# Kernel tuning notes

Hardware: AMD Instinct MI355X
Metric: run time of the kernel (lower is better)

Reference implementation:

```python
import jax, jax.numpy as jnp
import numpy as np

B, L, D = 2, 2048, 512
DI, N, K, R = 1024, 16, 4, 32  # d_inner=2*d_model, d_state, d_conv, dt_rank=ceil(512/16)
CK = 31   # conformer depthwise kernel
DFF = 2048  # feedforward_factor * d_hidden

def _ln(h, g, b):
    m = h.mean(-1, keepdims=True)
    v = ((h - m) ** 2).mean(-1, keepdims=True)
    return (h - m) * jax.lax.rsqrt(v + 1e-5) * g + b

def _dwconv(h, w, b, pad):
    # h: [B,L,C], w: [C,1,K] depthwise kernel
    y = jax.lax.conv_general_dilated(h.transpose(0, 2, 1), w, (1,), [pad],
                                     feature_group_count=h.shape[-1],
                                     dimension_numbers=('NCH', 'OIH', 'NCH'))
    return y.transpose(0, 2, 1) + b

def setup_inputs():
    key = jax.random.key(0)
    ks = jax.random.split(key, 16)
    nrm = lambda k, s, sc=0.02: jax.random.normal(k, s, jnp.float32) * sc
    return {
        'x': jax.random.normal(ks[0], (B, L, D), jnp.float32),
        'ln_g': jnp.ones(D), 'ln_b': jnp.zeros(D),
        'W_in': nrm(ks[1], (D, 2 * DI)),
        'conv_w': nrm(ks[2], (DI, 1, K), 0.1), 'conv_b': jnp.zeros(DI),
        'W_x': nrm(ks[3], (DI, R + 2 * N)),
        'W_dt': nrm(ks[4], (R, DI), 0.1), 'b_dt': nrm(ks[5], (DI,), 0.1),
        'A_log': jnp.log(jnp.broadcast_to(jnp.arange(1, N + 1, dtype=jnp.float32), (DI, N))),
        'Dp': jnp.ones(DI),
        'W_out': nrm(ks[6], (DI, D)),
        'cm_ln_g': jnp.ones(D), 'cm_ln_b': jnp.zeros(D),
        'cm_pw1_w': nrm(ks[7], (D, 2 * D)), 'cm_pw1_b': jnp.zeros(2 * D),
        'cm_dw_w': nrm(ks[8], (D, 1, CK), 0.1), 'cm_dw_b': jnp.zeros(D),
        'cm_pw2_w': nrm(ks[9], (D, D)), 'cm_pw2_b': jnp.zeros(D),
        'ff_W1': nrm(ks[10], (D, DFF)), 'ff_b1': jnp.zeros(DFF),
        'ff_W2': nrm(ks[11], (DFF, D)), 'ff_b2': jnp.zeros(D),
    }

def _forward(x, ln_g, ln_b, W_in, conv_w, conv_b, W_x, W_dt, b_dt, A_log, Dp, W_out,
             cm_ln_g, cm_ln_b, cm_pw1_w, cm_pw1_b, cm_dw_w, cm_dw_b, cm_pw2_w, cm_pw2_b,
             ff_W1, ff_b1, ff_W2, ff_b2):
    # --- pre LayerNorm ---
    h = _ln(x, ln_g, ln_b)
    # --- Mamba block ---
    xz = h @ W_in                       # [B,L,2*DI]
    xi, z = xz[..., :DI], xz[..., DI:]
    xc = jax.nn.silu(_dwconv(xi, conv_w, conv_b, (K - 1, 0)))  # causal depthwise conv
    dbl = xc @ W_x                      # [B,L,R+2N]
    dt, Bm, Cm = dbl[..., :R], dbl[..., R:R + N], dbl[..., R + N:]
    delta = jax.nn.softplus(dt @ W_dt + b_dt)           # [B,L,DI]
    A = -jnp.exp(A_log)                                  # [DI,N]
    dA = jnp.exp(delta[..., None] * A)                   # [B,L,DI,N]
    dBu = (delta * xc)[..., None] * Bm[:, :, None, :]    # [B,L,DI,N]
    def step(hs, inp):
        a, bu, c = inp
        hs = a * hs + bu                                 # [B,DI,N]
        return hs, jnp.einsum('bdn,bn->bd', hs, c)
    h0 = jnp.zeros((x.shape[0], DI, N), x.dtype)
    _, ys = jax.lax.scan(step, h0, (dA.transpose(1, 0, 2, 3), dBu.transpose(1, 0, 2, 3), Cm.transpose(1, 0, 2)))
    y = ys.transpose(1, 0, 2) + Dp * xc
    y = y * jax.nn.silu(z)
    m = y @ W_out                                        # [B,L,D]
    # --- Conformer-style conv module (residual) ---
    c = _ln(m, cm_ln_g, cm_ln_b)
    c = c @ cm_pw1_w + cm_pw1_b
    a_, g_ = jnp.split(c, 2, axis=-1)
    c = a_ * jax.nn.sigmoid(g_)  # GLU
    c = jax.nn.silu(_dwconv(c, cm_dw_w, cm_dw_b, ((CK - 1) // 2, (CK - 1) // 2)))
    c = c @ cm_pw2_w + cm_pw2_b
    m = m + c
    # --- post LayerNorm (shared params) + FFN (residual) ---
    f = _ln(m, ln_g, ln_b)
    out = f + (jax.nn.gelu(f @ ff_W1 + ff_b1) @ ff_W2 + ff_b2)
    return out

def reference(x, ln_g, ln_b, W_in, conv_w, conv_b, W_x, W_dt, b_dt, A_log, Dp, W_out,
              cm_ln_g, cm_ln_b, cm_pw1_w, cm_pw1_b, cm_dw_w, cm_dw_b, cm_pw2_w, cm_pw2_b,
              ff_W1, ff_b1, ff_W2, ff_b2):
    return _forward(x, ln_g, ln_b, W_in, conv_w, conv_b, W_x, W_dt, b_dt, A_log, Dp, W_out,
                    cm_ln_g, cm_ln_b, cm_pw1_w, cm_pw1_b, cm_dw_w, cm_dw_b, cm_pw2_w, cm_pw2_b,
                    ff_W1, ff_b1, ff_W2, ff_b2)
```

## Files before the change

### kernel.cpp

```cpp
#include <hip/hip_runtime.h>
#include <hip/hip_bf16.h>
#include <math.h>

#define Bc   2
#define Lc   2048
#define Dc   512
#define DIc  1024
#define Nc   16
#define Kc   4
#define Rc   32
#define CKc  31
#define DFFc 2048
#define Mrows (Bc*Lc)
#define CHUNK  32
#define NCHUNK 64

typedef __hip_bfloat16 bf16;
typedef short bf16x8 __attribute__((ext_vector_type(8)));
typedef float f32x4  __attribute__((ext_vector_type(4)));

__device__ __forceinline__ float sigmoidf_(float x){ return 1.f/(1.f+expf(-x)); }
__device__ __forceinline__ float siluf_(float x){ return x*sigmoidf_(x); }
__device__ __forceinline__ float softplusf_(float x){ return fmaxf(x,0.f)+log1pf(expf(-fabsf(x))); }
__device__ __forceinline__ float geluf_(float x){
    float x3 = x*x*x;
    return 0.5f*x*(1.f+tanhf(0.7978845608028654f*(x+0.044715f*x3)));
}

__device__ __forceinline__ void gload16(const void* g, void* l) {
    __builtin_amdgcn_global_load_lds((const __attribute__((address_space(1))) void*)g,
                                     (__attribute__((address_space(3))) void*)l, 16, 0, 0);
}

template<bool WF, bool WB>
__global__ void ln_kernel(const float* __restrict__ in, const float* __restrict__ g,
                          const float* __restrict__ bb, float* __restrict__ outf,
                          bf16* __restrict__ outb, int D) {
    int row = blockIdx.x;
    const float* x = in + (size_t)row * D;
    float s = 0.f, s2 = 0.f;
    for (int i = threadIdx.x; i < D; i += blockDim.x) { float v = x[i]; s += v; s2 += v*v; }
    #pragma unroll
    for (int off = 32; off; off >>= 1) { s += __shfl_down(s, off); s2 += __shfl_down(s2, off); }
    __shared__ float sh[2][4];
    int wave = threadIdx.x >> 6, lane = threadIdx.x & 63;
    if (lane == 0) { sh[0][wave] = s; sh[1][wave] = s2; }
    __syncthreads();
    if (threadIdx.x == 0) {
        float ts = 0.f, ts2 = 0.f;
        int nw = blockDim.x >> 6;
        for (int w = 0; w < nw; ++w) { ts += sh[0][w]; ts2 += sh[1][w]; }
        sh[0][0] = ts; sh[1][0] = ts2;
    }
    __syncthreads();
    float mean = sh[0][0] / D;
    float var  = sh[1][0] / D - mean*mean;
    float rstd = rsqrtf(var + 1e-5f);
    for (int i = threadIdx.x; i < D; i += blockDim.x) {
        float v = (x[i]-mean)*rstd*g[i] + bb[i];
        if (WF) outf[(size_t)row*D + i] = v;
        if (WB) outb[(size_t)row*D + i] = __float2bfloat16(v);
    }
}

struct WtPack {
    const float* W[8];
    bf16* Wt[8];
    int K[8];
    int N[8];
    int start[9];
};

__global__ void wtrans_all(WtPack p) {
    __shared__ float t[32][33];
    int tb = blockIdx.x;
    int wi = 0;
    #pragma unroll
    for (int i = 0; i < 7; ++i) if (tb >= p.start[i+1]) wi = i+1;
    int lt = tb - p.start[wi];
    int K = p.K[wi], N = p.N[wi];
    int ntx = N >> 5;
    int bx = lt % ntx, by = lt / ntx;
    const float* W = p.W[wi];
    bf16* Wt = p.Wt[wi];
    int tx = threadIdx.x, ty = threadIdx.y;
    #pragma unroll
    for (int i = 0; i < 32; i += 8)
        t[ty+i][tx] = W[(size_t)(by*32+ty+i)*N + bx*32+tx];
    __syncthreads();
    #pragma unroll
    for (int i = 0; i < 32; i += 8)
        Wt[(size_t)(bx*32+ty+i)*K + by*32+tx] = __float2bfloat16(t[tx][ty+i]);
}

template<int BM, int BN, int SPLITK, int ZSEL, int ACT, bool BIAS, bool RES, bool WF32, bool WBF16>
__global__ __launch_bounds__(256) void mgemm(const bf16* __restrict__ A, int lda,
                                             const bf16* __restrict__ Wt,
                                             const float* __restrict__ bias,
                                             const float* __restrict__ res,
                                             float* __restrict__ outf,
                                             bf16* __restrict__ outb,
                                             int M, int N, int K) {
    constexpr int BK = 32;
    constexpr int WM = BM/2, WN = BN/2;
    constexpr int AM = WM/16, AN = WN/16;
    constexpr int AISS = BM/64, BISS = BN/64;
    __shared__ __align__(16) bf16 As[2][BM*BK];
    __shared__ __align__(16) bf16 Bs[2][BN*BK];
    const int tid  = threadIdx.x;
    const int wave = tid >> 6, lane = tid & 63;
    const int r16  = lane & 15, kb = lane >> 4;
    const int gx = gridDim.x;
    const int nwg = gx*gridDim.y;
    const int id  = blockIdx.y*gx + blockIdx.x;
    const int sid = (id & 7)*(nwg >> 3) + (id >> 3);
    const int bm = (sid / gx)*BM, bn = (sid % gx)*BN;
    const int wm = (wave>>1)*WM, wn = (wave&1)*WN;
    const bf16* Wp = Wt;
    float* outfp = outf;
    bf16*  outbp = outb;
    if (ZSEL) {
        Wp += (size_t)blockIdx.z*N*K;
        if (WF32)  outfp += (size_t)blockIdx.z*M*N;
        if (WBF16) outbp += (size_t)blockIdx.z*M*N;
    }
    const int Keff = K / SPLITK;
    const int kz0  = (SPLITK > 1) ? blockIdx.z * Keff : 0;
    f32x4 acc[AM][AN] = {};
    const int nt = Keff / BK;

    auto stage = [&](int buf, int kt) {
        #pragma unroll
        for (int it = 0; it < AISS; ++it) {
            int base = (wave*AISS + it) << 10;
            int Lb   = base + (lane << 4);
            int row  = Lb >> 6;
            int gch  = ((Lb >> 4) & 3) ^ (row & 3);
            gload16(A + (size_t)(bm + row)*lda + kz0 + kt*BK + gch*8, (char*)As[buf] + base);
        }
        #pragma unroll
        for (int it = 0; it < BISS; ++it) {
            int base = (wave*BISS + it) << 10;
            int Lb   = base + (lane << 4);
            int row  = Lb >> 6;
            int gch  = ((Lb >> 4) & 3) ^ (row & 3);
            gload16(Wp + (size_t)(bn + row)*K + kz0 + kt*BK + gch*8, (char*)Bs[buf] + base);
        }
    };

    stage(0, 0);
    __syncthreads();
    for (int t = 0; t < nt; ++t) {
        int cur = t & 1;
        if (t + 1 < nt) stage(cur ^ 1, t + 1);
        bf16x8 af[AM], bfr[AN];
        #pragma unroll
        for (int mi = 0; mi < AM; ++mi) {
            int r = wm + mi*16 + r16;
            af[mi] = *(const bf16x8*)((const char*)As[cur] + r*64 + ((kb ^ (r & 3)) << 4));
        }
        #pragma unroll
        for (int ni = 0; ni < AN; ++ni) {
            int r = wn + ni*16 + r16;
            bfr[ni] = *(const bf16x8*)((const char*)Bs[cur] + r*64 + ((kb ^ (r & 3)) << 4));
        }
        #pragma unroll
        for (int mi = 0; mi < AM; ++mi)
            #pragma unroll
            for (int ni = 0; ni < AN; ++ni)
                acc[mi][ni] = __builtin_amdgcn_mfma_f32_16x16x32_bf16(af[mi], bfr[ni], acc[mi][ni], 0, 0, 0);
        __syncthreads();
    }

    #pragma unroll
    for (int mi = 0; mi < AM; ++mi) {
        #pragma unroll
        for (int ni = 0; ni < AN; ++ni) {
            #pragma unroll
            for (int r = 0; r < 4; ++r) {
                int grow = bm + wm + mi*16 + kb*4 + r;
                int gcol = bn + wn + ni*16 + r16;
                float v = acc[mi][ni][r];
                if (SPLITK > 1) {
                    outf[(size_t)blockIdx.z*M*N + (size_t)grow*N + gcol] = v;
                } else {
                    if (BIAS) v += bias[gcol];
                    if (ACT == 1) v = softplusf_(v);
                    else if (ACT == 2) v = geluf_(v);
                    if (RES) v += res[(size_t)grow*N + gcol];
                    if (WF32)  outfp[(size_t)grow*N + gcol] = v;
                    if (WBF16) outbp[(size_t)grow*N + gcol] = __float2bfloat16(v);
                }
            }
        }
    }
}

__global__ void splitk_combine(const float* __restrict__ part, float* __restrict__ outf,
                               bf16* __restrict__ outb, int n, int parts) {
    int i = blockIdx.x*256 + threadIdx.x;
    if (i >= n) return;
    float s = 0.f;
    for (int p = 0; p < parts; ++p) s += part[(size_t)p*n + i];
    outf[i] = s;
    outb[i] = __float2bfloat16(s);
}

template<int T>
__global__ __launch_bounds__(256) void causal_conv_silu(const bf16* __restrict__ xi, const float* __restrict__ w,
                                                        const float* __restrict__ bias,
                                                        bf16* __restrict__ xcb) {
    int d  = blockIdx.x*256 + threadIdx.x;
    int b  = blockIdx.y;
    int l0 = blockIdx.z*T;
    const bf16* src = xi + (size_t)b*Lc*DIc + d;
    float wt[Kc];
    #pragma unroll
    for (int k = 0; k < Kc; ++k) wt[k] = w[d*Kc + k];
    float win[T + Kc - 1];
    #pragma unroll
    for (int i = 0; i < T + Kc - 1; ++i) {
        int li = l0 - (Kc-1) + i;
        win[i] = (li >= 0) ? __bfloat162float(src[(size_t)li*DIc]) : 0.f;
    }
    float bv = bias[d];
    size_t obase = (size_t)b*Lc*DIc + (size_t)l0*DIc + d;
    #pragma unroll
    for (int o = 0; o < T; ++o) {
        float acc = bv;
        #pragma unroll
        for (int k = 0; k < Kc; ++k) acc = fmaf(win[o+k], wt[k], acc);
        xcb[obase + (size_t)o*DIc] = __float2bfloat16(siluf_(acc));
    }
}

__global__ __launch_bounds__(256) void scan_pass1(const float* __restrict__ delta, const bf16* __restrict__ xc,
                                                  const float* __restrict__ dbl, const float* __restrict__ A_log,
                                                  float* __restrict__ P, float* __restrict__ H) {
    int dgroup = blockIdx.x & 3;
    int bc = blockIdx.x >> 2;
    int b = bc & 1, chunk = bc >> 1;
    int d = dgroup*256 + threadIdx.x;
    float Av[16];
    #pragma unroll
    for (int j = 0; j < 4; ++j) {
        f32x4 v = *(const f32x4*)(&A_log[d*16 + 4*j]);
        #pragma unroll
        for (int q = 0; q < 4; ++q) Av[4*j+q] = -__expf(v[q]);
    }
    float h[16], Pl[16];
    #pragma unroll
    for (int n = 0; n < 16; ++n) { h[n] = 0.f; Pl[n] = 1.f; }
    size_t row0 = (size_t)b*Lc + (size_t)chunk*CHUNK;
    for (int i = 0; i < CHUNK; ++i) {
        size_t rowi = row0 + i;
        float dv  = delta[rowi*DIc + d];
        float xcv = __bfloat162float(xc[rowi*DIc + d]);
        float dxc = dv*xcv;
        f32x4 B0 = *(const f32x4*)(&dbl[rowi*64 + Rc + 0]);
        f32x4 B1 = *(const f32x4*)(&dbl[rowi*64 + Rc + 4]);
        f32x4 B2 = *(const f32x4*)(&dbl[rowi*64 + Rc + 8]);
        f32x4 B3 = *(const f32x4*)(&dbl[rowi*64 + Rc + 12]);
        float Bv[16];
        #pragma unroll
        for (int q = 0; q < 4; ++q) { Bv[q]=B0[q]; Bv[4+q]=B1[q]; Bv[8+q]=B2[q]; Bv[12+q]=B3[q]; }
        #pragma unroll
        for (int n = 0; n < 16; ++n) {
            float a = __expf(dv*Av[n]);
            h[n] = fmaf(a, h[n], dxc*Bv[n]);
            Pl[n] *= a;
        }
    }
    size_t pidx = ((size_t)chunk*2048 + (size_t)b*DIc + d) * 16;
    #pragma unroll
    for (int j = 0; j < 4; ++j) {
        f32x4 vp, vh;
        #pragma unroll
        for (int q = 0; q < 4; ++q) { vp[q] = Pl[4*j+q]; vh[q] = h[4*j+q]; }
        *(f32x4*)(&P[pidx + 4*j]) = vp;
        *(f32x4*)(&H[pidx + 4*j]) = vh;
    }
}

__global__ void scan_combine(float* __restrict__ P, const float* __restrict__ H) {
    int t = blockIdx.x*blockDim.x + threadIdx.x;
    float h = 0.f;
    #pragma unroll
    for (int c = 0; c < NCHUNK; ++c) {
        size_t idx = (size_t)c*32768 + t;
        float Pv = P[idx], Hv = H[idx];
        P[idx] = h;
        h = fmaf(Pv, h, Hv);
    }
}

__global__ __launch_bounds__(256) void scan_pass3(const float* __restrict__ delta, const bf16* __restrict__ xc,
                                                  const float* __restrict__ dbl, const bf16* __restrict__ z,
                                                  const float* __restrict__ A_log, const float* __restrict__ Dp,
                                                  const float* __restrict__ hstart, bf16* __restrict__ y) {
    int dgroup = blockIdx.x & 3;
    int bc = blockIdx.x >> 2;
    int b = bc & 1, chunk = bc >> 1;
    int d = dgroup*256 + threadIdx.x;
    float Av[16];
    #pragma unroll
    for (int j = 0; j < 4; ++j) {
        f32x4 v = *(const f32x4*)(&A_log[d*16 + 4*j]);
        #pragma unroll
        for (int q = 0; q < 4; ++q) Av[4*j+q] = -__expf(v[q]);
    }
    float Dv = Dp[d];
    float h[16];
    size_t pidx = ((size_t)chunk*2048 + (size_t)b*DIc + d) * 16;
    #pragma unroll
    for (int j = 0; j < 4; ++j) {
        f32x4 v = *(const f32x4*)(&hstart[pidx + 4*j]);
        #pragma unroll
        for (int q = 0; q < 4; ++q) h[4*j+q] = v[q];
    }
    size_t row0 = (size_t)b*Lc + (size_t)chunk*CHUNK;
    for (int i = 0; i < CHUNK; ++i) {
        size_t rowi = row0 + i;
        float dv  = delta[rowi*DIc + d];
        float xcv = __bfloat162float(xc[rowi*DIc + d]);
        float dxc = dv*xcv;
        f32x4 B0 = *(const f32x4*)(&dbl[rowi*64 + Rc + 0]);
        f32x4 B1 = *(const f32x4*)(&dbl[rowi*64 + Rc + 4]);
        f32x4 B2 = *(const f32x4*)(&dbl[rowi*64 + Rc + 8]);
        f32x4 B3 = *(const f32x4*)(&dbl[rowi*64 + Rc + 12]);
        f32x4 C0 = *(const f32x4*)(&dbl[rowi*64 + Rc + Nc + 0]);
        f32x4 C1 = *(const f32x4*)(&dbl[rowi*64 + Rc + Nc + 4]);
        f32x4 C2 = *(const f32x4*)(&dbl[rowi*64 + Rc + Nc + 8]);
        f32x4 C3 = *(const f32x4*)(&dbl[rowi*64 + Rc + Nc + 12]);
        float Bv[16], Cv[16];
        #pragma unroll
        for (int q = 0; q < 4; ++q) {
            Bv[q]=B0[q]; Bv[4+q]=B1[q]; Bv[8+q]=B2[q]; Bv[12+q]=B3[q];
            Cv[q]=C0[q]; Cv[4+q]=C1[q]; Cv[8+q]=C2[q]; Cv[12+q]=C3[q];
        }
        float s0=0.f, s1=0.f, s2=0.f, s3=0.f;
        #pragma unroll
        for (int n = 0; n < 16; ++n) {
            float a = __expf(dv*Av[n]);
            h[n] = fmaf(a, h[n], dxc*Bv[n]);
        }
        #pragma unroll
        for (int j = 0; j < 4; ++j) {
            s0 = fmaf(h[4*j+0], Cv[4*j+0], s0);
            s1 = fmaf(h[4*j+1], Cv[4*j+1], s1);
            s2 = fmaf(h[4*j+2], Cv[4*j+2], s2);
            s3 = fmaf(h[4*j+3], Cv[4*j+3], s3);
        }
        float contrib = (s0+s1)+(s2+s3);
        float zv = __bfloat162float(z[rowi*DIc + d]);
        y[rowi*DIc + d] = __float2bfloat16((contrib + Dv*xcv) * siluf_(zv));
    }
}

template<int T>
__global__ __launch_bounds__(256) void sym_conv_glu_silu(const bf16* __restrict__ c2, const float* __restrict__ w,
                                                         const float* __restrict__ bias, bf16* __restrict__ out) {
    int d  = blockIdx.x*256 + threadIdx.x;
    int b  = blockIdx.y;
    int l0 = blockIdx.z*T;
    const bf16* base = c2 + (size_t)b*Lc*(2*Dc) + d;
    float wt[CKc];
    #pragma unroll
    for (int k = 0; k < CKc; ++k) wt[k] = w[d*CKc + k];
    constexpr int HALF = (CKc-1)/2;
    float win[T + CKc - 1];
    #pragma unroll
    for (int i = 0; i < T + CKc - 1; ++i) {
        int li = l0 - HALF + i;
        if (li >= 0 && li < Lc) {
            float a = __bfloat162float(base[(size_t)li*(2*Dc)]);
            float g = __bfloat162float(base[(size_t)li*(2*Dc) + Dc]);
            win[i] = a * sigmoidf_(g);
        } else win[i] = 0.f;
    }
    float bv = bias[d];
    size_t obase = (size_t)b*Lc*Dc + (size_t)l0*Dc + d;
    #pragma unroll
    for (int o = 0; o < T; ++o) {
        float acc = bv;
        #pragma unroll
        for (int k = 0; k < CKc; ++k) acc = fmaf(win[o+k], wt[k], acc);
        out[obase + (size_t)o*Dc] = __float2bfloat16(siluf_(acc));
    }
}

extern "C" void kernel_launch(void* const* d_in, const int* in_sizes, int n_in,
                              void* d_out, int out_size, void* d_ws, size_t ws_size,
                              hipStream_t stream) {
    const float* x      = (const float*)d_in[0];
    const float* ln_g   = (const float*)d_in[1];
    const float* ln_b   = (const float*)d_in[2];
    const float* W_in   = (const float*)d_in[3];
    const float* conv_w = (const float*)d_in[4];
    const float* conv_b = (const float*)d_in[5];
    const float* W_x    = (const float*)d_in[6];
    const float* W_dt   = (const float*)d_in[7];
    const float* b_dt   = (const float*)d_in[8];
    const float* A_log  = (const float*)d_in[9];
    const float* Dp     = (const float*)d_in[10];
    const float* W_out  = (const float*)d_in[11];
    const float* cm_ln_g= (const float*)d_in[12];
    const float* cm_ln_b= (const float*)d_in[13];
    const float* pw1_w  = (const float*)d_in[14];
    const float* pw1_b  = (const float*)d_in[15];
    const float* dw_w   = (const float*)d_in[16];
    const float* dw_b   = (const float*)d_in[17];
    const float* pw2_w  = (const float*)d_in[18];
    const float* pw2_b  = (const float*)d_in[19];
    const float* ff_W1  = (const float*)d_in[20];
    const float* ff_b1  = (const float*)d_in[21];
    const float* ff_W2  = (const float*)d_in[22];
    const float* ff_b2  = (const float*)d_in[23];
    float* out = (float*)d_out;
    float* ws  = (float*)d_ws;

    float* A_  = ws;
    float* A2_ = ws + 4194304;
    float* B_  = ws + 8388608;
    float* C_  = ws + 12582912;
    float* D_  = ws + 12845056;
    float* F_  = ws + 17039360;
    float* H_  = ws + 18612224;
    float* J_  = ws + 20709376;

    bf16*  xib     = (bf16*)A_;
    bf16*  zb      = xib + (size_t)Mrows*DIc;
    float* part_buf= A_;
    bf16*  c2b     = (bf16*)A_;
    float* P_buf   = A2_;
    float* H_buf   = A2_ + 2097152;
    bf16*  g1b     = (bf16*)B_;
    float* dbl_buf = C_;
    float* dl_buf  = D_;
    float* m_buf   = D_;
    bf16*  dblb    = (bf16*)F_;
    bf16*  cb      = (bf16*)F_;
    bf16*  ccb     = (bf16*)F_;
    bf16*  fb      = (bf16*)F_;
    bf16*  hb      = (bf16*)H_;
    bf16*  xcb     = (bf16*)H_;
    bf16*  yb      = (bf16*)H_;
    float* f_buf   = out;

    bf16* Jw = (bf16*)J_;
    bf16* Win_t  = Jw;
    bf16* Wx_t   = Jw + 1048576;
    bf16* Wdt_t  = Jw + 1114112;
    bf16* Wout_t = Jw + 1146880;
    bf16* pw1_t  = Jw + 1671168;
    bf16* pw2_t  = Jw + 2195456;
    bf16* ffW1_t = Jw + 2457600;
    bf16* ffW2_t = Jw + 3506176;

    const int M = Mrows;

    {
        WtPack p;
        const float* Ws[8] = {W_in, W_x, W_dt, W_out, pw1_w, pw2_w, ff_W1, ff_W2};
        bf16* Ts[8] = {Win_t, Wx_t, Wdt_t, Wout_t, pw1_t, pw2_t, ffW1_t, ffW2_t};
        int Ks[8] = {512, 1024, 32, 1024, 512, 512, 512, 2048};
        int Ns[8] = {2048, 64, 1024, 512, 1024, 512, 2048, 512};
        int acc = 0;
        for (int i = 0; i < 8; ++i) {
            p.W[i] = Ws[i]; p.Wt[i] = Ts[i]; p.K[i] = Ks[i]; p.N[i] = Ns[i];
            p.start[i] = acc;
            acc += (Ns[i]/32)*(Ks[i]/32);
        }
        p.start[8] = acc;
        wtrans_all<<<acc, dim3(32,8), 0, stream>>>(p);
    }

    ln_kernel<false,true><<<M, 256, 0, stream>>>(x, ln_g, ln_b, nullptr, hb, Dc);
    mgemm<128,64,1,1,0,false,false,false,true><<<dim3(1024/64, M/128, 2), 256, 0, stream>>>(
        hb, Dc, Win_t, nullptr, nullptr, nullptr, xib, M, DIc, Dc);
    causal_conv_silu<16><<<dim3(DIc/256, Bc, Lc/16), 256, 0, stream>>>(xib, conv_w, conv_b, xcb);
    mgemm<64,64,8,0,0,false,false,true,false><<<dim3(64/64, M/64, 8), 256, 0, stream>>>(
        xcb, DIc, Wx_t, nullptr, nullptr, part_buf, nullptr, M, 64, DIc);
    splitk_combine<<<(M*64+255)/256, 256, 0, stream>>>(part_buf, dbl_buf, dblb, M*64, 8);
    mgemm<64,64,1,0,1,true,false,true,false><<<dim3(1024/64, M/64), 256, 0, stream>>>(
        dblb, 64, Wdt_t, b_dt, nullptr, dl_buf, nullptr, M, DIc, Rc);
    scan_pass1<<<512, 256, 0, stream>>>(dl_buf, xcb, dbl_buf, A_log, P_buf, H_buf);
    scan_combine<<<128, 256, 0, stream>>>(P_buf, H_buf);
    scan_pass3<<<512, 256, 0, stream>>>(dl_buf, xcb, dbl_buf, zb, A_log, Dp, P_buf, yb);
    mgemm<64,64,1,0,0,false,false,true,false><<<dim3(512/64, M/64), 256, 0, stream>>>(
        yb, DIc, Wout_t, nullptr, nullptr, m_buf, nullptr, M, Dc, DIc);
    ln_kernel<false,true><<<M, 256, 0, stream>>>(m_buf, cm_ln_g, cm_ln_b, nullptr, cb, Dc);
    mgemm<128,64,1,0,0,true,false,false,true><<<dim3(1024/64, M/128), 256, 0, stream>>>(
        cb, Dc, pw1_t, pw1_b, nullptr, nullptr, c2b, M, 2*Dc, Dc);
    sym_conv_glu_silu<16><<<dim3(Dc/256, Bc, Lc/16), 256, 0, stream>>>(c2b, dw_w, dw_b, ccb);
    mgemm<64,64,1,0,0,true,true,true,false><<<dim3(512/64, M/64), 256, 0, stream>>>(
        ccb, Dc, pw2_t, pw2_b, m_buf, m_buf, nullptr, M, Dc, Dc);
    ln_kernel<true,true><<<M, 256, 0, stream>>>(m_buf, ln_g, ln_b, f_buf, fb, Dc);
    mgemm<128,64,1,0,2,true,false,false,true><<<dim3(2048/64, M/128), 256, 0, stream>>>(
        fb, Dc, ffW1_t, ff_b1, nullptr, nullptr, g1b, M, DFFc, Dc);
    mgemm<64,64,1,0,0,true,true,true,false><<<dim3(512/64, M/64), 256, 0, stream>>>(
        g1b, DFFc, ffW2_t, ff_b2, f_buf, out, nullptr, M, Dc, DFFc);
}
```

Before: 251.7 us.

## Fold W_x·W_dt into one composed weight and merge prep kernels

Precomputes the product of the dt slice of W_x with W_dt and stacks it with the B/C columns of W_x (plus zero padding) into one 1088-column bf16 weight. A single GEMM over xc then yields softplus(delta) and B/C directly, replacing the split-K x_proj GEMM, the combine kernel and the dt GEMM. The first LayerNorm is also folded into the weight-prep launch. The trade-off is a larger GEMM, with K=1024 over 1088 columns instead of 32 columns for the dt projection. The dt path also skips the bf16 rounding of the rank-32 intermediate, which slightly changes numerics.

Measured after the change: 277.0 us. 1.1x slower.

```diff
diff --git a/kernel.cpp b/kernel.cpp
--- a/kernel.cpp
+++ b/kernel.cpp
@@ -63,37 +63,76 @@
     }
 }
 
-struct WtPack {
-    const float* W[8];
-    bf16* Wt[8];
-    int K[8];
-    int N[8];
-    int start[9];
+struct PrepPack {
+    const float* W[6]; bf16* Wt[6]; int K[6]; int N[6]; int start[7];
+    const float* Wx; const float* Wdt; bf16* Wsc;
+    const float* x; const float* lg; const float* lb; bf16* hb;
+    int compStart, bcStart, zeroStart, lnStart;
 };
 
-__global__ void wtrans_all(WtPack p) {
+__global__ __launch_bounds__(256) void prep_all(PrepPack p) {
     __shared__ float t[32][33];
-    int tb = blockIdx.x;
-    int wi = 0;
-    #pragma unroll
-    for (int i = 0; i < 7; ++i) if (tb >= p.start[i+1]) wi = i+1;
-    int lt = tb - p.start[wi];
-    int K = p.K[wi], N = p.N[wi];
-    int ntx = N >> 5;
-    int bx = lt % ntx, by = lt / ntx;
-    const float* W = p.W[wi];
-    bf16* Wt = p.Wt[wi];
-    int tx = threadIdx.x, ty = threadIdx.y;
-    #pragma unroll
-    for (int i = 0; i < 32; i += 8)
-        t[ty+i][tx] = W[(size_t)(by*32+ty+i)*N + bx*32+tx];
-    __syncthreads();
-    #pragma unroll
-    for (int i = 0; i < 32; i += 8)
-        Wt[(size_t)(bx*32+ty+i)*K + by*32+tx] = __float2bfloat16(t[tx][ty+i]);
-}
-
-template<int BM, int BN, int SPLITK, int ZSEL, int ACT, bool BIAS, bool RES, bool WF32, bool WBF16>
+    __shared__ float sh[2][4];
+    int tb = blockIdx.x, tid = threadIdx.x;
+    if (tb < p.compStart) {
+        int wi = 0;
+        #pragma unroll
+        for (int i = 0; i < 5; ++i) if (tb >= p.start[i+1]) wi = i+1;
+        int lt = tb - p.start[wi];
+        int K = p.K[wi], N = p.N[wi];
+        int ntx = N >> 5;
+        int bx = lt % ntx, by = lt / ntx;
+        const float* W = p.W[wi];
+        bf16* Wt = p.Wt[wi];
+        int tx = tid & 31, ty = tid >> 5;
+        #pragma unroll
+        for (int i = 0; i < 32; i += 8)
+            t[ty+i][tx] = W[(size_t)(by*32+ty+i)*N + bx*32+tx];
+        __syncthreads();
+        #pragma unroll
+        for (int i = 0; i < 32; i += 8)
+            Wt[(size_t)(bx*32+ty+i)*K + by*32+tx] = __float2bfloat16(t[tx][ty+i]);
+    } else if (tb < p.bcStart) {
+        int idx = (tb - p.compStart)*256 + tid;
+        int n = idx >> 10, k = idx & 1023;
+        float s = 0.f;
+        #pragma unroll
+        for (int r = 0; r < 32; ++r)
+            s = fmaf(p.Wx[k*64 + r], p.Wdt[r*1024 + n], s);
+        p.Wsc[(size_t)n*1024 + k] = __float2bfloat16(s);
+    } else if (tb < p.zeroStart) {
+        int idx = (tb - p.bcStart)*256 + tid;
+        int j = idx >> 10, k = idx & 1023;
+        p.Wsc[(size_t)(1024+j)*1024 + k] = __float2bfloat16(p.Wx[k*64 + 32 + j]);
+    } else if (tb < p.lnStart) {
+        int idx = (tb - p.zeroStart)*256 + tid;
+        int j = idx >> 10, k = idx & 1023;
+        p.Wsc[(size_t)(1056+j)*1024 + k] = __float2bfloat16(0.f);
+    } else {
+        int row = tb - p.lnStart;
+        const float* xr = p.x + (size_t)row * Dc;
+        float s = 0.f, s2 = 0.f;
+        for (int i = tid; i < Dc; i += 256) { float v = xr[i]; s += v; s2 += v*v; }
+        #pragma unroll
+        for (int off = 32; off; off >>= 1) { s += __shfl_down(s, off); s2 += __shfl_down(s2, off); }
+        int wave = tid >> 6, lane = tid & 63;
+        if (lane == 0) { sh[0][wave] = s; sh[1][wave] = s2; }
+        __syncthreads();
+        if (tid == 0) {
+            float ts = 0.f, ts2 = 0.f;
+            for (int w = 0; w < 4; ++w) { ts += sh[0][w]; ts2 += sh[1][w]; }
+            sh[0][0] = ts; sh[1][0] = ts2;
+        }
+        __syncthreads();
+        float mean = sh[0][0] / Dc;
+        float var  = sh[1][0] / Dc - mean*mean;
+        float rstd = rsqrtf(var + 1e-5f);
+        for (int i = tid; i < Dc; i += 256)
+            p.hb[(size_t)row*Dc + i] = __float2bfloat16((xr[i]-mean)*rstd*p.lg[i] + p.lb[i]);
+    }
+}
+
+template<int BM, int BN, int ZSEL, int ACT, bool BIAS, bool RES, bool WF32, bool WBF16, bool SCANEP>
 __global__ __launch_bounds__(256) void mgemm(const bf16* __restrict__ A, int lda,
                                              const bf16* __restrict__ Wt,
                                              const float* __restrict__ bias,
@@ -124,10 +163,8 @@
         if (WF32)  outfp += (size_t)blockIdx.z*M*N;
         if (WBF16) outbp += (size_t)blockIdx.z*M*N;
     }
-    const int Keff = K / SPLITK;
-    const int kz0  = (SPLITK > 1) ? blockIdx.z * Keff : 0;
     f32x4 acc[AM][AN] = {};
-    const int nt = Keff / BK;
+    const int nt = K / BK;
 
     auto stage = [&](int buf, int kt) {
         #pragma unroll
@@ -136,7 +173,7 @@
             int Lb   = base + (lane << 4);
             int row  = Lb >> 6;
             int gch  = ((Lb >> 4) & 3) ^ (row & 3);
-            gload16(A + (size_t)(bm + row)*lda + kz0 + kt*BK + gch*8, (char*)As[buf] + base);
+            gload16(A + (size_t)(bm + row)*lda + kt*BK + gch*8, (char*)As[buf] + base);
         }
         #pragma unroll
         for (int it = 0; it < BISS; ++it) {
@@ -144,7 +181,7 @@
             int Lb   = base + (lane << 4);
             int row  = Lb >> 6;
             int gch  = ((Lb >> 4) & 3) ^ (row & 3);
-            gload16(Wp + (size_t)(bn + row)*K + kz0 + kt*BK + gch*8, (char*)Bs[buf] + base);
+            gload16(Wp + (size_t)(bn + row)*K + kt*BK + gch*8, (char*)Bs[buf] + base);
         }
     };
 
@@ -181,8 +218,12 @@
                 int grow = bm + wm + mi*16 + kb*4 + r;
                 int gcol = bn + wn + ni*16 + r16;
                 float v = acc[mi][ni][r];
-                if (SPLITK > 1) {
-                    outf[(size_t)blockIdx.z*M*N + (size_t)grow*N + gcol] = v;
+                if (SCANEP) {
+                    if (gcol < 1024) {
+                        outf[(size_t)grow*1024 + gcol] = softplusf_(v + bias[gcol]);
+                    } else if (gcol < 1056) {
+                        ((float*)outb)[(size_t)grow*32 + (gcol - 1024)] = v;
+                    }
                 } else {
                     if (BIAS) v += bias[gcol];
                     if (ACT == 1) v = softplusf_(v);
@@ -196,16 +237,6 @@
     }
 }
 
-__global__ void splitk_combine(const float* __restrict__ part, float* __restrict__ outf,
-                               bf16* __restrict__ outb, int n, int parts) {
-    int i = blockIdx.x*256 + threadIdx.x;
-    if (i >= n) return;
-    float s = 0.f;
-    for (int p = 0; p < parts; ++p) s += part[(size_t)p*n + i];
-    outf[i] = s;
-    outb[i] = __float2bfloat16(s);
-}
-
 template<int T>
 __global__ __launch_bounds__(256) void causal_conv_silu(const bf16* __restrict__ xi, const float* __restrict__ w,
                                                         const float* __restrict__ bias,
@@ -235,11 +266,11 @@
 }
 
 __global__ __launch_bounds__(256) void scan_pass1(const float* __restrict__ delta, const bf16* __restrict__ xc,
-                                                  const float* __restrict__ dbl, const float* __restrict__ A_log,
+                                                  const float* __restrict__ bc, const float* __restrict__ A_log,
                                                   float* __restrict__ P, float* __restrict__ H) {
     int dgroup = blockIdx.x & 3;
-    int bc = blockIdx.x >> 2;
-    int b = bc & 1, chunk = bc >> 1;
+    int bci = blockIdx.x >> 2;
+    int b = bci & 1, chunk = bci >> 1;
     int d = dgroup*256 + threadIdx.x;
     float Av[16];
     #pragma unroll
@@ -257,10 +288,10 @@
         float dv  = delta[rowi*DIc + d];
         float xcv = __bfloat162float(xc[rowi*DIc + d]);
         float dxc = dv*xcv;
-        f32x4 B0 = *(const f32x4*)(&dbl[rowi*64 + Rc + 0]);
-        f32x4 B1 = *(const f32x4*)(&dbl[rowi*64 + Rc + 4]);
-        f32x4 B2 = *(const f32x4*)(&dbl[rowi*64 + Rc + 8]);
-        f32x4 B3 = *(const f32x4*)(&dbl[rowi*64 + Rc + 12]);
+        f32x4 B0 = *(const f32x4*)(&bc[rowi*32 + 0]);
+        f32x4 B1 = *(const f32x4*)(&bc[rowi*32 + 4]);
+        f32x4 B2 = *(const f32x4*)(&bc[rowi*32 + 8]);
+        f32x4 B3 = *(const f32x4*)(&bc[rowi*32 + 12]);
         float Bv[16];
         #pragma unroll
         for (int q = 0; q < 4; ++q) { Bv[q]=B0[q]; Bv[4+q]=B1[q]; Bv[8+q]=B2[q]; Bv[12+q]=B3[q]; }
@@ -295,12 +326,12 @@
 }
 
 __global__ __launch_bounds__(256) void scan_pass3(const float* __restrict__ delta, const bf16* __restrict__ xc,
-                                                  const float* __restrict__ dbl, const bf16* __restrict__ z,
+                                                  const float* __restrict__ bc, const bf16* __restrict__ z,
                                                   const float* __restrict__ A_log, const float* __restrict__ Dp,
                                                   const float* __restrict__ hstart, bf16* __restrict__ y) {
     int dgroup = blockIdx.x & 3;
-    int bc = blockIdx.x >> 2;
-    int b = bc & 1, chunk = bc >> 1;
+    int bci = blockIdx.x >> 2;
+    int b = bci & 1, chunk = bci >> 1;
     int d = dgroup*256 + threadIdx.x;
     float Av[16];
     #pragma unroll
@@ -324,14 +355,14 @@
         float dv  = delta[rowi*DIc + d];
         float xcv = __bfloat162float(xc[rowi*DIc + d]);
         float dxc = dv*xcv;
-        f32x4 B0 = *(const f32x4*)(&dbl[rowi*64 + Rc + 0]);
-        f32x4 B1 = *(const f32x4*)(&dbl[rowi*64 + Rc + 4]);
-        f32x4 B2 = *(const f32x4*)(&dbl[rowi*64 + Rc + 8]);
-        f32x4 B3 = *(const f32x4*)(&dbl[rowi*64 + Rc + 12]);
-        f32x4 C0 = *(const f32x4*)(&dbl[rowi*64 + Rc + Nc + 0]);
-        f32x4 C1 = *(const f32x4*)(&dbl[rowi*64 + Rc + Nc + 4]);
-        f32x4 C2 = *(const f32x4*)(&dbl[rowi*64 + Rc + Nc + 8]);
-        f32x4 C3 = *(const f32x4*)(&dbl[rowi*64 + Rc + Nc + 12]);
+        f32x4 B0 = *(const f32x4*)(&bc[rowi*32 + 0]);
+        f32x4 B1 = *(const f32x4*)(&bc[rowi*32 + 4]);
+        f32x4 B2 = *(const f32x4*)(&bc[rowi*32 + 8]);
+        f32x4 B3 = *(const f32x4*)(&bc[rowi*32 + 12]);
+        f32x4 C0 = *(const f32x4*)(&bc[rowi*32 + 16]);
+        f32x4 C1 = *(const f32x4*)(&bc[rowi*32 + 20]);
+        f32x4 C2 = *(const f32x4*)(&bc[rowi*32 + 24]);
+        f32x4 C3 = *(const f32x4*)(&bc[rowi*32 + 28]);
         float Bv[16], Cv[16];
         #pragma unroll
         for (int q = 0; q < 4; ++q) {
@@ -430,15 +461,14 @@
 
     bf16*  xib     = (bf16*)A_;
     bf16*  zb      = xib + (size_t)Mrows*DIc;
-    float* part_buf= A_;
     bf16*  c2b     = (bf16*)A_;
+    bf16*  Wsc     = (bf16*)A2_;
     float* P_buf   = A2_;
     float* H_buf   = A2_ + 2097152;
     bf16*  g1b     = (bf16*)B_;
-    float* dbl_buf = C_;
+    float* bc_buf  = C_;
     float* dl_buf  = D_;
     float* m_buf   = D_;
-    bf16*  dblb    = (bf16*)F_;
     bf16*  cb      = (bf16*)F_;
     bf16*  ccb     = (bf16*)F_;
     bf16*  fb      = (bf16*)F_;
@@ -449,55 +479,56 @@
 
     bf16* Jw = (bf16*)J_;
     bf16* Win_t  = Jw;
-    bf16* Wx_t   = Jw + 1048576;
-    bf16* Wdt_t  = Jw + 1114112;
-    bf16* Wout_t = Jw + 1146880;
-    bf16* pw1_t  = Jw + 1671168;
-    bf16* pw2_t  = Jw + 2195456;
-    bf16* ffW1_t = Jw + 2457600;
-    bf16* ffW2_t = Jw + 3506176;
+    bf16* Wout_t = Jw + 1048576;
+    bf16* pw1_t  = Jw + 1572864;
+    bf16* pw2_t  = Jw + 2097152;
+    bf16* ffW1_t = Jw + 2359296;
+    bf16* ffW2_t = Jw + 3407872;
 
     const int M = Mrows;
 
     {
-        WtPack p;
-        const float* Ws[8] = {W_in, W_x, W_dt, W_out, pw1_w, pw2_w, ff_W1, ff_W2};
-        bf16* Ts[8] = {Win_t, Wx_t, Wdt_t, Wout_t, pw1_t, pw2_t, ffW1_t, ffW2_t};
-        int Ks[8] = {512, 1024, 32, 1024, 512, 512, 512, 2048};
-        int Ns[8] = {2048, 64, 1024, 512, 1024, 512, 2048, 512};
+        PrepPack p;
+        const float* Ws[6] = {W_in, W_out, pw1_w, pw2_w, ff_W1, ff_W2};
+        bf16* Ts[6] = {Win_t, Wout_t, pw1_t, pw2_t, ffW1_t, ffW2_t};
+        int Ks[6] = {512, 1024, 512, 512, 512, 2048};
+        int Ns[6] = {2048, 512, 1024, 512, 2048, 512};
         int acc = 0;
-        for (int i = 0; i < 8; ++i) {
+        for (int i = 0; i < 6; ++i) {
             p.W[i] = Ws[i]; p.Wt[i] = Ts[i]; p.K[i] = Ks[i]; p.N[i] = Ns[i];
             p.start[i] = acc;
             acc += (Ns[i]/32)*(Ks[i]/32);
         }
-        p.start[8] = acc;
-        wtrans_all<<<acc, dim3(32,8), 0, stream>>>(p);
-    }
-
-    ln_kernel<false,true><<<M, 256, 0, stream>>>(x, ln_g, ln_b, nullptr, hb, Dc);
-    mgemm<128,64,1,1,0,false,false,false,true><<<dim3(1024/64, M/128, 2), 256, 0, stream>>>(
+        p.start[6] = acc;
+        p.compStart = acc;
+        p.bcStart   = acc + 4096;
+        p.zeroStart = p.bcStart + 128;
+        p.lnStart   = p.zeroStart + 128;
+        int total   = p.lnStart + M;
+        p.Wx = W_x; p.Wdt = W_dt; p.Wsc = Wsc;
+        p.x = x; p.lg = ln_g; p.lb = ln_b; p.hb = hb;
+        prep_all<<<total, 256, 0, stream>>>(p);
+    }
+
+    mgemm<128,64,1,0,false,false,false,true,false><<<dim3(1024/64, M/128, 2), 256, 0, stream>>>(
         hb, Dc, Win_t, nullptr, nullptr, nullptr, xib, M, DIc, Dc);
     causal_conv_silu<16><<<dim3(DIc/256, Bc, Lc/16), 256, 0, stream>>>(xib, conv_w, conv_b, xcb);
-    mgemm<64,64,8,0,0,false,false,true,false><<<dim3(64/64, M/64, 8), 256, 0, stream>>>(
-        xcb, DIc, Wx_t, nullptr, nullptr, part_buf, nullptr, M, 64, DIc);
-    splitk_combine<<<(M*64+255)/256, 256, 0, stream>>>(part_buf, dbl_buf, dblb, M*64, 8);
-    mgemm<64,64,1,0,1,true,false,true,false><<<dim3(1024/64, M/64), 256, 0, stream>>>(
-        dblb, 64, Wdt_t, b_dt, nullptr, dl_buf, nullptr, M, DIc, Rc);
-    scan_pass1<<<512, 256, 0, stream>>>(dl_buf, xcb, dbl_buf, A_log, P_buf, H_buf);
+    mgemm<128,64,0,0,false,false,false,false,true><<<dim3(1088/64, M/128), 256, 0, stream>>>(
+        xcb, DIc, Wsc, b_dt, nullptr, dl_buf, (bf16*)bc_buf, M, 1088, DIc);
+    scan_pass1<<<512, 256, 0, stream>>>(dl_buf, xcb, bc_buf, A_log, P_buf, H_buf);
     scan_combine<<<128, 256, 0, stream>>>(P_buf, H_buf);
-    scan_pass3<<<512, 256, 0, stream>>>(dl_buf, xcb, dbl_buf, zb, A_log, Dp, P_buf, yb);
-    mgemm<64,64,1,0,0,false,false,true,false><<<dim3(512/64, M/64), 256, 0, stream>>>(
+    scan_pass3<<<512, 256, 0, stream>>>(dl_buf, xcb, bc_buf, zb, A_log, Dp, P_buf, yb);
+    mgemm<64,64,0,0,false,false,true,false,false><<<dim3(512/64, M/64), 256, 0, stream>>>(
         yb, DIc, Wout_t, nullptr, nullptr, m_buf, nullptr, M, Dc, DIc);
     ln_kernel<false,true><<<M, 256, 0, stream>>>(m_buf, cm_ln_g, cm_ln_b, nullptr, cb, Dc);
-    mgemm<128,64,1,0,0,true,false,false,true><<<dim3(1024/64, M/128), 256, 0, stream>>>(
+    mgemm<128,64,0,0,true,false,false,true,false><<<dim3(1024/64, M/128), 256, 0, stream>>>(
         cb, Dc, pw1_t, pw1_b, nullptr, nullptr, c2b, M, 2*Dc, Dc);
     sym_conv_glu_silu<16><<<dim3(Dc/256, Bc, Lc/16), 256, 0, stream>>>(c2b, dw_w, dw_b, ccb);
-    mgemm<64,64,1,0,0,true,true,true,false><<<dim3(512/64, M/64), 256, 0, stream>>>(
+    mgemm<64,64,0,0,true,true,true,false,false><<<dim3(512/64, M/64), 256, 0, stream>>>(
         ccb, Dc, pw2_t, pw2_b, m_buf, m_buf, nullptr, M, Dc, Dc);
     ln_kernel<true,true><<<M, 256, 0, stream>>>(m_buf, ln_g, ln_b, f_buf, fb, Dc);
-    mgemm<128,64,1,0,2,true,false,false,true><<<dim3(2048/64, M/128), 256, 0, stream>>>(
+    mgemm<128,64,0,2,true,false,false,true,false><<<dim3(2048/64, M/128), 256, 0, stream>>>(
         fb, Dc, ffW1_t, ff_b1, nullptr, nullptr, g1b, M, DFFc, Dc);
-    mgemm<64,64,1,0,0,true,true,true,false><<<dim3(512/64, M/64), 256, 0, stream>>>(
+    mgemm<64,64,0,0,true,true,true,false,false><<<dim3(512/64, M/64), 256, 0, stream>>>(
         g1b, DFFc, ffW2_t, ff_b2, f_buf, out, nullptr, M, Dc, DFFc);
 }
```

## Add intra-block wave split-K GEMM for narrow-N layers and fuse prep kernels

Applied to the files above, without the earlier changes.

Adds a wgemm kernel where each of the four waves computes a quarter of K for a 64x64 tile, using its own double-buffered, swizzled LDS region. The four partial results are then reduced through LDS before the bias, residual and store epilogue. It replaces mgemm for the three N=512 GEMMs (W_out, pw2, ff_W2), aiming to shorten the K loop per wave and avoid cross-wave synchronisation inside the loop, at the cost of 64KB LDS per block and lower occupancy. It also folds the first LayerNorm into the weight-transpose launch to save one kernel launch.

After: 240.0 us. 1.05x faster.

```diff
diff --git a/kernel.cpp b/kernel.cpp
--- a/kernel.cpp
+++ b/kernel.cpp
@@ -63,34 +63,56 @@
     }
 }
 
-struct WtPack {
-    const float* W[8];
-    bf16* Wt[8];
-    int K[8];
-    int N[8];
-    int start[9];
+struct PrepPack {
+    const float* W[8]; bf16* Wt[8]; int K[8]; int N[8]; int start[9];
+    const float* x; const float* lg; const float* lb; bf16* hb;
+    int lnStart;
 };
 
-__global__ void wtrans_all(WtPack p) {
+__global__ __launch_bounds__(256) void prep_all(PrepPack p) {
     __shared__ float t[32][33];
-    int tb = blockIdx.x;
-    int wi = 0;
-    #pragma unroll
-    for (int i = 0; i < 7; ++i) if (tb >= p.start[i+1]) wi = i+1;
-    int lt = tb - p.start[wi];
-    int K = p.K[wi], N = p.N[wi];
-    int ntx = N >> 5;
-    int bx = lt % ntx, by = lt / ntx;
-    const float* W = p.W[wi];
-    bf16* Wt = p.Wt[wi];
-    int tx = threadIdx.x, ty = threadIdx.y;
-    #pragma unroll
-    for (int i = 0; i < 32; i += 8)
-        t[ty+i][tx] = W[(size_t)(by*32+ty+i)*N + bx*32+tx];
-    __syncthreads();
-    #pragma unroll
-    for (int i = 0; i < 32; i += 8)
-        Wt[(size_t)(bx*32+ty+i)*K + by*32+tx] = __float2bfloat16(t[tx][ty+i]);
+    __shared__ float sh[2][4];
+    int tb = blockIdx.x, tid = threadIdx.x;
+    if (tb < p.lnStart) {
+        int wi = 0;
+        #pragma unroll
+        for (int i = 0; i < 7; ++i) if (tb >= p.start[i+1]) wi = i+1;
+        int lt = tb - p.start[wi];
+        int K = p.K[wi], N = p.N[wi];
+        int ntx = N >> 5;
+        int bx = lt % ntx, by = lt / ntx;
+        const float* W = p.W[wi];
+        bf16* Wt = p.Wt[wi];
+        int tx = tid & 31, ty = tid >> 5;
+        #pragma unroll
+        for (int i = 0; i < 32; i += 8)
+            t[ty+i][tx] = W[(size_t)(by*32+ty+i)*N + bx*32+tx];
+        __syncthreads();
+        #pragma unroll
+        for (int i = 0; i < 32; i += 8)
+            Wt[(size_t)(bx*32+ty+i)*K + by*32+tx] = __float2bfloat16(t[tx][ty+i]);
+    } else {
+        int row = tb - p.lnStart;
+        const float* xr = p.x + (size_t)row * Dc;
+        float s = 0.f, s2 = 0.f;
+        for (int i = tid; i < Dc; i += 256) { float v = xr[i]; s += v; s2 += v*v; }
+        #pragma unroll
+        for (int off = 32; off; off >>= 1) { s += __shfl_down(s, off); s2 += __shfl_down(s2, off); }
+        int wave = tid >> 6, lane = tid & 63;
+        if (lane == 0) { sh[0][wave] = s; sh[1][wave] = s2; }
+        __syncthreads();
+        if (tid == 0) {
+            float ts = 0.f, ts2 = 0.f;
+            for (int w = 0; w < 4; ++w) { ts += sh[0][w]; ts2 += sh[1][w]; }
+            sh[0][0] = ts; sh[1][0] = ts2;
+        }
+        __syncthreads();
+        float mean = sh[0][0] / Dc;
+        float var  = sh[1][0] / Dc - mean*mean;
+        float rstd = rsqrtf(var + 1e-5f);
+        for (int i = tid; i < Dc; i += 256)
+            p.hb[(size_t)row*Dc + i] = __float2bfloat16((xr[i]-mean)*rstd*p.lg[i] + p.lb[i]);
+    }
 }
 
 template<int BM, int BN, int SPLITK, int ZSEL, int ACT, bool BIAS, bool RES, bool WF32, bool WBF16>
@@ -196,6 +218,108 @@
     }
 }
 
+template<int ACT, bool BIAS, bool RES, bool WF32, bool WBF16>
+__global__ __launch_bounds__(256) void wgemm(const bf16* __restrict__ A, int lda,
+                                             const bf16* __restrict__ Wt,
+                                             const float* __restrict__ bias,
+                                             const float* __restrict__ res,
+                                             float* __restrict__ outf,
+                                             bf16* __restrict__ outb,
+                                             int M, int N, int K) {
+    constexpr int BM = 64, BN = 64, BK = 32;
+    __shared__ __align__(16) char lds[65536];
+    const int tid  = threadIdx.x;
+    const int wave = tid >> 6, lane = tid & 63;
+    const int r16  = lane & 15, kb = lane >> 4;
+    const int gx = gridDim.x;
+    const int nwg = gx*gridDim.y;
+    const int id  = blockIdx.y*gx + blockIdx.x;
+    const int sid = (id & 7)*(nwg >> 3) + (id >> 3);
+    const int bm = (sid / gx)*BM, bn = (sid % gx)*BN;
+    const int Kw  = K >> 2;
+    const int k0w = wave * Kw;
+    const int nt  = Kw / BK;
+    char* myL = lds + wave*16384;
+    f32x4 acc[4][4] = {};
+
+    auto stage = [&](int buf, int kt) {
+        #pragma unroll
+        for (int it = 0; it < 4; ++it) {
+            int base = it << 10;
+            int Lb   = base + (lane << 4);
+            int row  = Lb >> 6;
+            int gch  = ((Lb >> 4) & 3) ^ (row & 3);
+            gload16(A + (size_t)(bm + row)*lda + k0w + kt*BK + gch*8, myL + buf*8192 + base);
+        }
+        #pragma unroll
+        for (int it = 0; it < 4; ++it) {
+            int base = it << 10;
+            int Lb   = base + (lane << 4);
+            int row  = Lb >> 6;
+            int gch  = ((Lb >> 4) & 3) ^ (row & 3);
+            gload16(Wt + (size_t)(bn + row)*K + k0w + kt*BK + gch*8, myL + buf*8192 + 4096 + base);
+        }
+    };
+
+    stage(0, 0);
+    for (int t = 0; t < nt; ++t) {
+        int cur = t & 1;
+        if (t + 1 < nt) {
+            stage(cur ^ 1, t + 1);
+            asm volatile("s_waitcnt vmcnt(8)" ::: "memory");
+        } else {
+            asm volatile("s_waitcnt vmcnt(0)" ::: "memory");
+        }
+        __builtin_amdgcn_sched_barrier(0);
+        const char* bufA = myL + cur*8192;
+        const char* bufB = bufA + 4096;
+        bf16x8 af[4], bfr[4];
+        #pragma unroll
+        for (int mi = 0; mi < 4; ++mi) {
+            int r = mi*16 + r16;
+            af[mi] = *(const bf16x8*)(bufA + r*64 + ((kb ^ (r & 3)) << 4));
+        }
+        #pragma unroll
+        for (int ni = 0; ni < 4; ++ni) {
+            int r = ni*16 + r16;
+            bfr[ni] = *(const bf16x8*)(bufB + r*64 + ((kb ^ (r & 3)) << 4));
+        }
+        #pragma unroll
+        for (int mi = 0; mi < 4; ++mi)
+            #pragma unroll
+            for (int ni = 0; ni < 4; ++ni)
+                acc[mi][ni] = __builtin_amdgcn_mfma_f32_16x16x32_bf16(af[mi], bfr[ni], acc[mi][ni], 0, 0, 0);
+    }
+
+    __syncthreads();
+    float* red = (float*)lds;
+    #pragma unroll
+    for (int mi = 0; mi < 4; ++mi) {
+        #pragma unroll
+        for (int ni = 0; ni < 4; ++ni) {
+            int row0 = mi*16 + kb*4;
+            int col  = ni*16 + r16;
+            #pragma unroll
+            for (int r = 0; r < 4; ++r)
+                red[wave*4096 + (row0+r)*64 + col] = acc[mi][ni][r];
+        }
+    }
+    __syncthreads();
+    #pragma unroll
+    for (int i = 0; i < 16; ++i) {
+        int o = i*256 + tid;
+        int row = o >> 6, col = o & 63;
+        float v = red[o] + red[4096+o] + red[8192+o] + red[12288+o];
+        int grow = bm + row, gcol = bn + col;
+        if (BIAS) v += bias[gcol];
+        if (ACT == 1) v = softplusf_(v);
+        else if (ACT == 2) v = geluf_(v);
+        if (RES) v += res[(size_t)grow*N + gcol];
+        if (WF32)  outf[(size_t)grow*N + gcol] = v;
+        if (WBF16) outb[(size_t)grow*N + gcol] = __float2bfloat16(v);
+    }
+}
+
 __global__ void splitk_combine(const float* __restrict__ part, float* __restrict__ outf,
                                bf16* __restrict__ outb, int n, int parts) {
     int i = blockIdx.x*256 + threadIdx.x;
@@ -238,8 +362,8 @@
                                                   const float* __restrict__ dbl, const float* __restrict__ A_log,
                                                   float* __restrict__ P, float* __restrict__ H) {
     int dgroup = blockIdx.x & 3;
-    int bc = blockIdx.x >> 2;
-    int b = bc & 1, chunk = bc >> 1;
+    int bci = blockIdx.x >> 2;
+    int b = bci & 1, chunk = bci >> 1;
     int d = dgroup*256 + threadIdx.x;
     float Av[16];
     #pragma unroll
@@ -299,8 +423,8 @@
                                                   const float* __restrict__ A_log, const float* __restrict__ Dp,
                                                   const float* __restrict__ hstart, bf16* __restrict__ y) {
     int dgroup = blockIdx.x & 3;
-    int bc = blockIdx.x >> 2;
-    int b = bc & 1, chunk = bc >> 1;
+    int bci = blockIdx.x >> 2;
+    int b = bci & 1, chunk = bci >> 1;
     int d = dgroup*256 + threadIdx.x;
     float Av[16];
     #pragma unroll
@@ -460,7 +584,7 @@
     const int M = Mrows;
 
     {
-        WtPack p;
+        PrepPack p;
         const float* Ws[8] = {W_in, W_x, W_dt, W_out, pw1_w, pw2_w, ff_W1, ff_W2};
         bf16* Ts[8] = {Win_t, Wx_t, Wdt_t, Wout_t, pw1_t, pw2_t, ffW1_t, ffW2_t};
         int Ks[8] = {512, 1024, 32, 1024, 512, 512, 512, 2048};
@@ -472,10 +596,11 @@
             acc += (Ns[i]/32)*(Ks[i]/32);
         }
         p.start[8] = acc;
-        wtrans_all<<<acc, dim3(32,8), 0, stream>>>(p);
-    }
-
-    ln_kernel<false,true><<<M, 256, 0, stream>>>(x, ln_g, ln_b, nullptr, hb, Dc);
+        p.lnStart = acc;
+        p.x = x; p.lg = ln_g; p.lb = ln_b; p.hb = hb;
+        prep_all<<<acc + M, 256, 0, stream>>>(p);
+    }
+
     mgemm<128,64,1,1,0,false,false,false,true><<<dim3(1024/64, M/128, 2), 256, 0, stream>>>(
         hb, Dc, Win_t, nullptr, nullptr, nullptr, xib, M, DIc, Dc);
     causal_conv_silu<16><<<dim3(DIc/256, Bc, Lc/16), 256, 0, stream>>>(xib, conv_w, conv_b, xcb);
@@ -487,17 +612,17 @@
     scan_pass1<<<512, 256, 0, stream>>>(dl_buf, xcb, dbl_buf, A_log, P_buf, H_buf);
     scan_combine<<<128, 256, 0, stream>>>(P_buf, H_buf);
     scan_pass3<<<512, 256, 0, stream>>>(dl_buf, xcb, dbl_buf, zb, A_log, Dp, P_buf, yb);
-    mgemm<64,64,1,0,0,false,false,true,false><<<dim3(512/64, M/64), 256, 0, stream>>>(
+    wgemm<0,false,false,true,false><<<dim3(512/64, M/64), 256, 0, stream>>>(
         yb, DIc, Wout_t, nullptr, nullptr, m_buf, nullptr, M, Dc, DIc);
     ln_kernel<false,true><<<M, 256, 0, stream>>>(m_buf, cm_ln_g, cm_ln_b, nullptr, cb, Dc);
     mgemm<128,64,1,0,0,true,false,false,true><<<dim3(1024/64, M/128), 256, 0, stream>>>(
         cb, Dc, pw1_t, pw1_b, nullptr, nullptr, c2b, M, 2*Dc, Dc);
     sym_conv_glu_silu<16><<<dim3(Dc/256, Bc, Lc/16), 256, 0, stream>>>(c2b, dw_w, dw_b, ccb);
-    mgemm<64,64,1,0,0,true,true,true,false><<<dim3(512/64, M/64), 256, 0, stream>>>(
+    wgemm<0,true,true,true,false><<<dim3(512/64, M/64), 256, 0, stream>>>(
         ccb, Dc, pw2_t, pw2_b, m_buf, m_buf, nullptr, M, Dc, Dc);
     ln_kernel<true,true><<<M, 256, 0, stream>>>(m_buf, ln_g, ln_b, f_buf, fb, Dc);
     mgemm<128,64,1,0,2,true,false,false,true><<<dim3(2048/64, M/128), 256, 0, stream>>>(
         fb, Dc, ffW1_t, ff_b1, nullptr, nullptr, g1b, M, DFFc, Dc);
-    mgemm<64,64,1,0,0,true,true,true,false><<<dim3(512/64, M/64), 256, 0, stream>>>(
+    wgemm<0,true,true,true,false><<<dim3(512/64, M/64), 256, 0, stream>>>(
         g1b, DFFc, ffW2_t, ff_b2, f_buf, out, nullptr, M, Dc, DFFc);
 }
```
